# Kernel tuning notes

Measured on AMD Instinct MI355X. Metric: run time of the kernel, lower is better.

The kernel has to match this reference:

```python
import jax, jax.numpy as jnp
import numpy as np

B, N, K = 256, 1024, 64          # batch, atoms per structure, abc combinations
E = 2 * K                        # embedding_dim = 128
NSG = 230                        # number of space groups
LN_EPS = 1e-5


def setup_inputs() -> dict:
    key = jax.random.key(0)
    ks = jax.random.split(key, 12)
    xav = float(np.sqrt(6.0 / (K + K)))  # xavier_uniform bound for [K,K] slices
    return {
        "atom_positions": jax.random.uniform(ks[0], (B, N, 3), dtype=jnp.float32),
        "reciprocal_matrices": jax.random.normal(ks[1], (B, 3, 3), dtype=jnp.float32),
        "space_group": jax.random.randint(ks[2], (B, 1), 1, NSG + 1, dtype=jnp.int32),
        "abc_combinations": jax.random.normal(ks[3], (K, 3), dtype=jnp.float32),
        "graphs_array": jax.random.uniform(ks[4], (NSG, K, K), dtype=jnp.float32),
        "w_real": jax.random.uniform(ks[5], (NSG, K, K), jnp.float32, -xav, xav),
        "w_imag": jax.random.uniform(ks[6], (NSG, K, K), jnp.float32, -xav, xav),
        "b_real": jnp.zeros((NSG, K), jnp.float32),
        "b_imag": jnp.zeros((NSG, K), jnp.float32),
        "W2": jax.random.normal(ks[7], (E, E), dtype=jnp.float32) * 0.05,
        "b2": jnp.zeros((E,), jnp.float32),
        "gamma": jnp.ones((E,), jnp.float32),
        "beta": jnp.zeros((E,), jnp.float32),
    }


def reference(atom_positions, reciprocal_matrices, space_group, abc_combinations,
              graphs_array, w_real, w_imag, b_real, b_imag, W2, b2, gamma, beta):
    sg = space_group[:, 0] - 1                                  # [B] in [0,229]
    # transformed_abc = abc @ recip^T : [B,K,3]
    t_abc = jnp.einsum('kc,bdc->bkd', abc_combinations, reciprocal_matrices)
    # encodings = exp(i*2pi * pos @ t_abc^T) : [B,N,K] complex
    phase = (2.0 * jnp.pi) * jnp.einsum('bnc,bkc->bnk', atom_positions, t_abc)
    enc = jax.lax.complex(jnp.cos(phase), jnp.sin(phase))
    # per-sample adjacency gather + complex batched matmul
    adj = graphs_array[sg]                                      # [B,K,K]
    weighted = jnp.einsum('bnk,bkm->bnm', enc, adj.astype(enc.dtype))
    weighted = weighted[:, :, :K]                               # slice to embedding_dim//2
    # SpaceGroupDenseLayer: per-sample complex expert weights
    Wc = jax.lax.complex(w_real, w_imag)[sg]                    # [B,K,K]
    bc = jax.lax.complex(b_real, b_imag)[sg][:, None, :]        # [B,1,K]
    out_c = jnp.einsum('bni,bif->bnf', weighted, Wc) + bc       # [B,N,K] complex
    x = jnp.concatenate([out_c.real, out_c.imag], axis=-1)      # [B,N,2K]
    x = jax.nn.silu(x)
    x = x @ W2.T + b2                                           # Linear(E,E)
    mu = jnp.mean(x, axis=-1, keepdims=True)
    var = jnp.mean(jnp.square(x - mu), axis=-1, keepdims=True)
    return (x - mu) * jax.lax.rsqrt(var + LN_EPS) * gamma + beta
```

## Files before the change

### kernel.cpp

```cpp
#include <hip/hip_runtime.h>
#include <math.h>

#define BB 256
#define NN 1024
#define KK 64
#define EE 128
#define TM 128

typedef _Float16 half8 __attribute__((ext_vector_type(8)));
typedef float f32x4 __attribute__((ext_vector_type(4)));

__device__ __forceinline__ int swz(int row, int halfcol) {
    return (row * EE + halfcol) ^ ((row & 7) << 3);
}
__device__ __forceinline__ int swzX(int row, int halfcol) {
    return (row * EE + halfcol) ^ (((row >> 2) & 3) << 4);
}

__device__ __forceinline__ void gload_lds16(const void* g, void* l) {
    __builtin_amdgcn_global_load_lds(
        (const __attribute__((address_space(1))) unsigned int*)g,
        (__attribute__((address_space(3))) unsigned int*)l, 16, 0, 0);
}

__global__ __launch_bounds__(256) void prep_kernel(
    const float* __restrict__ recip,
    const int* __restrict__ space_group,
    const float* __restrict__ abc,
    const float* __restrict__ graphs,
    const float* __restrict__ w_real,
    const float* __restrict__ w_imag,
    const float* __restrict__ b_real,
    const float* __restrict__ b_imag,
    const float* __restrict__ W2,
    _Float16* __restrict__ Mt,
    float* __restrict__ bbout,
    float* __restrict__ tabcP,
    _Float16* __restrict__ W2h)
{
    const int b = blockIdx.x;
    const int t = threadIdx.x;
    const int sg = space_group[b] - 1;

    if (b < EE * EE / 256) {
        const int idx = b * 256 + t;
        W2h[idx] = (_Float16)W2[idx];
    }

    __shared__ float adjL[KK * KK];
    __shared__ float wrL[KK * KK];
    __shared__ float wiL[KK * KK];

    const float* adjG = graphs + (size_t)sg * KK * KK;
    const float* wrG  = w_real + (size_t)sg * KK * KK;
    const float* wiG  = w_imag + (size_t)sg * KK * KK;
    for (int idx = t; idx < KK * KK; idx += 256) {
        adjL[idx] = adjG[idx];
        wrL[idx]  = wrG[idx];
        wiL[idx]  = wiG[idx];
    }
    __syncthreads();

    const int i  = t >> 2;
    const int f0 = (t & 3) * 16;
    float cr[16], ci[16];
#pragma unroll
    for (int c = 0; c < 16; ++c) { cr[c] = 0.f; ci[c] = 0.f; }
    for (int k = 0; k < KK; ++k) {
        const float a = adjL[i * KK + k];
#pragma unroll
        for (int c = 0; c < 16; ++c) {
            cr[c] += a * wrL[k * KK + f0 + c];
            ci[c] += a * wiL[k * KK + f0 + c];
        }
    }
    _Float16* Mb = Mt + (size_t)b * EE * EE;
#pragma unroll
    for (int c = 0; c < 16; ++c) {
        const int f = f0 + c;
        Mb[f * EE + i]             = (_Float16)cr[c];
        Mb[f * EE + KK + i]        = (_Float16)(-ci[c]);
        Mb[(KK + f) * EE + i]      = (_Float16)ci[c];
        Mb[(KK + f) * EE + KK + i] = (_Float16)cr[c];
    }
    if (t < EE) {
        bbout[b * EE + t] = (t < KK) ? b_real[sg * KK + t] : b_imag[sg * KK + (t - KK)];
    }
    if (t < KK) {
        const float a0 = abc[t * 3 + 0], a1 = abc[t * 3 + 1], a2 = abc[t * 3 + 2];
        const float* R = recip + b * 9;
        float4 v;
        v.x = a0 * R[0] + a1 * R[1] + a2 * R[2];
        v.y = a0 * R[3] + a1 * R[4] + a2 * R[5];
        v.z = a0 * R[6] + a1 * R[7] + a2 * R[8];
        v.w = 0.f;
        *(float4*)&tabcP[((size_t)b * KK + t) * 4] = v;
    }
}

__global__ __launch_bounds__(512, 4) void main_kernel(
    const float* __restrict__ pos,
    const _Float16* __restrict__ Mt,
    const float* __restrict__ bball,
    const float* __restrict__ tabcP,
    const _Float16* __restrict__ W2h,
    const float* __restrict__ b2,
    const float* __restrict__ gamma,
    const float* __restrict__ beta,
    float* __restrict__ out)
{
    const int d = blockIdx.x;
    const int j   = d >> 3;
    const int b   = (d & 7) * 32 + (j >> 3);
    const int seg = j & 7;
    const int n0  = seg * TM;
    const int t  = threadIdx.x;
    const int w    = t >> 6;
    const int lane = t & 63;
    const int ln15 = lane & 15;
    const int kg   = lane >> 4;

    __shared__ __align__(16) _Float16 arena[2 * EE * EE];
    _Float16* Bt = arena;
    _Float16* X  = arena + EE * EE;

    {
        const char* srcM = (const char*)(Mt + (size_t)b * EE * EE);
#pragma unroll
        for (int i = 0; i < 4; ++i) {
            const int c16 = t + i * 512;
            const int row = c16 >> 4;
            const int sl  = c16 & 15;
            const int g   = row * 16 + (sl ^ (row & 7));
            gload_lds16(srcM + g * 16, (char*)Bt + c16 * 16);
        }
    }

    const int grow = n0 + w * 16 + ln15;
    const float* pr = pos + ((size_t)b * NN + grow) * 3;
    const float px = pr[0], py = pr[1], pz = pr[2];
    const float* tp = tabcP + (size_t)b * KK * 4;

    half8 afrag[4];
#pragma unroll
    for (int mq = 0; mq < 2; ++mq) {
        _Float16 cb[8], sb[8];
#pragma unroll
        for (int jj = 0; jj < 8; ++jj) {
            const int k = mq * 32 + kg * 8 + jj;
            const float4 tv = *(const float4*)&tp[k * 4];
            const float rev = px * tv.x + py * tv.y + pz * tv.z;
            const float fr  = __builtin_amdgcn_fractf(rev);
            sb[jj] = (_Float16)__builtin_amdgcn_sinf(fr);
            cb[jj] = (_Float16)__builtin_amdgcn_cosf(fr);
        }
        afrag[mq]     = *(half8*)cb;
        afrag[mq + 2] = *(half8*)sb;
    }
    __syncthreads();

    f32x4 acc[8];
#pragma unroll
    for (int nt = 0; nt < 8; ++nt) {
        const int n = nt * 16 + ln15;
        f32x4 a = {0.f, 0.f, 0.f, 0.f};
#pragma unroll
        for (int kc = 0; kc < 4; ++kc) {
            const half8 bf = *(const half8*)&Bt[swz(n, kc * 32 + kg * 8)];
            a = __builtin_amdgcn_mfma_f32_16x16x32_f16(afrag[kc], bf, a, 0, 0, 0);
        }
        acc[nt] = a;
    }
    __syncthreads();

    {
        const char* srcW = (const char*)W2h;
#pragma unroll
        for (int i = 0; i < 4; ++i) {
            const int c16 = t + i * 512;
            const int row = c16 >> 4;
            const int sl  = c16 & 15;
            const int g   = row * 16 + (sl ^ (row & 7));
            gload_lds16(srcW + g * 16, (char*)Bt + c16 * 16);
        }
    }

#pragma unroll
    for (int nt = 0; nt < 8; ++nt) {
        const int col = nt * 16 + ln15;
        const float bbv = bball[b * EE + col];
#pragma unroll
        for (int r2 = 0; r2 < 4; ++r2) {
            const float v = acc[nt][r2] + bbv;
            const int rr = w * 16 + kg * 4 + r2;
            X[swzX(rr, col)] = (_Float16)(v / (1.f + __expf(-v)));
        }
    }

    const int arow = w * 16 + ln15;
    half8 a2[4];
#pragma unroll
    for (int kc = 0; kc < 4; ++kc)
        a2[kc] = *(const half8*)&X[swzX(arow, kc * 32 + kg * 8)];
    __syncthreads();

    f32x4 acc2[8];
#pragma unroll
    for (int nt = 0; nt < 8; ++nt) {
        const int n = nt * 16 + ln15;
        f32x4 a = {0.f, 0.f, 0.f, 0.f};
#pragma unroll
        for (int kc = 0; kc < 4; ++kc) {
            const half8 bf = *(const half8*)&Bt[swz(n, kc * 32 + kg * 8)];
            a = __builtin_amdgcn_mfma_f32_16x16x32_f16(a2[kc], bf, a, 0, 0, 0);
        }
        acc2[nt] = a;
    }

    float s[4] = {0.f, 0.f, 0.f, 0.f}, q[4] = {0.f, 0.f, 0.f, 0.f};
#pragma unroll
    for (int nt = 0; nt < 8; ++nt) {
        const int col = nt * 16 + ln15;
        const float b2v = b2[col];
#pragma unroll
        for (int r2 = 0; r2 < 4; ++r2) {
            const float v = acc2[nt][r2] + b2v;
            acc2[nt][r2] = v;
            s[r2] += v;
            q[r2] += v * v;
        }
    }
#pragma unroll
    for (int m = 1; m < 16; m <<= 1) {
#pragma unroll
        for (int r2 = 0; r2 < 4; ++r2) {
            s[r2] += __shfl_xor(s[r2], m);
            q[r2] += __shfl_xor(q[r2], m);
        }
    }
    const float inv = 1.f / EE;
    float mu[4], rs[4];
#pragma unroll
    for (int r2 = 0; r2 < 4; ++r2) {
        mu[r2] = s[r2] * inv;
        rs[r2] = rsqrtf(fmaxf(q[r2] * inv - mu[r2] * mu[r2], 0.f) + 1e-5f);
    }
#pragma unroll
    for (int nt = 0; nt < 8; ++nt) {
        const int col = nt * 16 + ln15;
        const float g  = gamma[col];
        const float be = beta[col];
#pragma unroll
        for (int r2 = 0; r2 < 4; ++r2) {
            const int rr = w * 16 + kg * 4 + r2;
            __builtin_nontemporal_store(
                (acc2[nt][r2] - mu[r2]) * rs[r2] * g + be,
                &out[((size_t)b * NN + n0 + rr) * EE + col]);
        }
    }
}

extern "C" void kernel_launch(void* const* d_in, const int* in_sizes, int n_in,
                              void* d_out, int out_size, void* d_ws, size_t ws_size,
                              hipStream_t stream) {
    const float* pos    = (const float*)d_in[0];
    const float* recip  = (const float*)d_in[1];
    const int*   sgp    = (const int*)d_in[2];
    const float* abc    = (const float*)d_in[3];
    const float* graphs = (const float*)d_in[4];
    const float* wr     = (const float*)d_in[5];
    const float* wi     = (const float*)d_in[6];
    const float* br     = (const float*)d_in[7];
    const float* bi     = (const float*)d_in[8];
    const float* W2     = (const float*)d_in[9];
    const float* b2     = (const float*)d_in[10];
    const float* gm     = (const float*)d_in[11];
    const float* bt     = (const float*)d_in[12];
    float* out = (float*)d_out;

    char* ws = (char*)d_ws;
    _Float16* Mt    = (_Float16*)ws;
    char* p = ws + (size_t)BB * EE * EE * 2;
    _Float16* W2h   = (_Float16*)p;            p += EE * EE * 2;
    float*    bball = (float*)p;               p += (size_t)BB * EE * 4;
    float*    tabcP = (float*)p;

    hipLaunchKernelGGL(prep_kernel, dim3(BB), dim3(256), 0, stream,
                       recip, sgp, abc, graphs, wr, wi, br, bi, W2, Mt, bball, tabcP, W2h);
    hipLaunchKernelGGL(main_kernel, dim3(BB * NN / TM), dim3(512), 0, stream,
                       pos, Mt, bball, tabcP, W2h, b2, gm, bt, out);
}
```

Baseline: 76.43 us.

## Split fused kernel into two matmul kernels with global fp16 intermediate

Splits the fused encoding+matmul+SiLU+matmul+LayerNorm kernel into two kernels that exchange the SiLU output through a 64 MB fp16 workspace buffer. The old fused kernel is kept as a fallback when the workspace is too small. This reduces per-kernel LDS and register pressure and removes the mid-kernel barrier with its W2 reload. The cost is a full extra global write and read of the intermediate, plus one more launch. It also changes the X swizzle and replaces the nontemporal output stores with plain stores.

```diff
diff --git a/kernel.cpp b/kernel.cpp
--- a/kernel.cpp
+++ b/kernel.cpp
@@ -12,9 +12,6 @@
 
 __device__ __forceinline__ int swz(int row, int halfcol) {
     return (row * EE + halfcol) ^ ((row & 7) << 3);
-}
-__device__ __forceinline__ int swzX(int row, int halfcol) {
-    return (row * EE + halfcol) ^ (((row >> 2) & 3) << 4);
 }
 
 __device__ __forceinline__ void gload_lds16(const void* g, void* l) {
@@ -98,7 +95,188 @@
     }
 }
 
-__global__ __launch_bounds__(512, 4) void main_kernel(
+__device__ __forceinline__ void block_map(int d, int& b, int& n0) {
+    const int j = d >> 3;
+    b  = (d & 7) * 32 + (j >> 3);
+    n0 = (j & 7) * TM;
+}
+
+__device__ __forceinline__ void make_afrag(const float* tp, float px, float py, float pz,
+                                           int kg, half8 afrag[4]) {
+#pragma unroll
+    for (int mq = 0; mq < 2; ++mq) {
+        _Float16 cb[8], sb[8];
+#pragma unroll
+        for (int jj = 0; jj < 8; ++jj) {
+            const int k = mq * 32 + kg * 8 + jj;
+            const float4 tv = *(const float4*)&tp[k * 4];
+            const float rev = px * tv.x + py * tv.y + pz * tv.z;
+            const float fr  = __builtin_amdgcn_fractf(rev);
+            sb[jj] = (_Float16)__builtin_amdgcn_sinf(fr);
+            cb[jj] = (_Float16)__builtin_amdgcn_cosf(fr);
+        }
+        afrag[mq]     = *(half8*)cb;
+        afrag[mq + 2] = *(half8*)sb;
+    }
+}
+
+__global__ __launch_bounds__(512) void mm1_kernel(
+    const float* __restrict__ pos,
+    const _Float16* __restrict__ Mt,
+    const float* __restrict__ bball,
+    const float* __restrict__ tabcP,
+    _Float16* __restrict__ Xg)
+{
+    int b, n0;
+    block_map(blockIdx.x, b, n0);
+    const int t  = threadIdx.x;
+    const int w    = t >> 6;
+    const int lane = t & 63;
+    const int ln15 = lane & 15;
+    const int kg   = lane >> 4;
+
+    __shared__ __align__(16) _Float16 Bt[EE * EE];
+
+    {
+        const char* srcM = (const char*)(Mt + (size_t)b * EE * EE);
+#pragma unroll
+        for (int i = 0; i < 4; ++i) {
+            const int c16 = t + i * 512;
+            const int row = c16 >> 4;
+            const int sl  = c16 & 15;
+            const int g   = row * 16 + (sl ^ (row & 7));
+            gload_lds16(srcM + g * 16, (char*)Bt + c16 * 16);
+        }
+    }
+
+    const int grow = n0 + w * 16 + ln15;
+    const float* pr = pos + ((size_t)b * NN + grow) * 3;
+    const float px = pr[0], py = pr[1], pz = pr[2];
+    half8 afrag[4];
+    make_afrag(tabcP + (size_t)b * KK * 4, px, py, pz, kg, afrag);
+    __syncthreads();
+
+    f32x4 acc[8];
+#pragma unroll
+    for (int nt = 0; nt < 8; ++nt) {
+        const int n = nt * 16 + ln15;
+        f32x4 a = {0.f, 0.f, 0.f, 0.f};
+#pragma unroll
+        for (int kc = 0; kc < 4; ++kc) {
+            const half8 bf = *(const half8*)&Bt[swz(n, kc * 32 + kg * 8)];
+            a = __builtin_amdgcn_mfma_f32_16x16x32_f16(afrag[kc], bf, a, 0, 0, 0);
+        }
+        acc[nt] = a;
+    }
+
+#pragma unroll
+    for (int nt = 0; nt < 8; ++nt) {
+        const int col = nt * 16 + ln15;
+        const float bbv = bball[b * EE + col];
+#pragma unroll
+        for (int r2 = 0; r2 < 4; ++r2) {
+            const float v = acc[nt][r2] + bbv;
+            const int rr = w * 16 + kg * 4 + r2;
+            Xg[((size_t)b * NN + n0 + rr) * EE + col] =
+                (_Float16)(v / (1.f + __expf(-v)));
+        }
+    }
+}
+
+__global__ __launch_bounds__(512) void mm2_kernel(
+    const _Float16* __restrict__ Xg,
+    const _Float16* __restrict__ W2h,
+    const float* __restrict__ b2,
+    const float* __restrict__ gamma,
+    const float* __restrict__ beta,
+    float* __restrict__ out)
+{
+    int b, n0;
+    block_map(blockIdx.x, b, n0);
+    const int t  = threadIdx.x;
+    const int w    = t >> 6;
+    const int lane = t & 63;
+    const int ln15 = lane & 15;
+    const int kg   = lane >> 4;
+
+    __shared__ __align__(16) _Float16 Bt[EE * EE];
+
+    const int grow = n0 + w * 16 + ln15;
+    const _Float16* xrow = Xg + ((size_t)b * NN + grow) * EE;
+    half8 a2[4];
+#pragma unroll
+    for (int kc = 0; kc < 4; ++kc)
+        a2[kc] = *(const half8*)&xrow[kc * 32 + kg * 8];
+
+    {
+        const char* srcW = (const char*)W2h;
+#pragma unroll
+        for (int i = 0; i < 4; ++i) {
+            const int c16 = t + i * 512;
+            const int row = c16 >> 4;
+            const int sl  = c16 & 15;
+            const int g   = row * 16 + (sl ^ (row & 7));
+            gload_lds16(srcW + g * 16, (char*)Bt + c16 * 16);
+        }
+    }
+    __syncthreads();
+
+    f32x4 acc2[8];
+#pragma unroll
+    for (int nt = 0; nt < 8; ++nt) {
+        const int n = nt * 16 + ln15;
+        f32x4 a = {0.f, 0.f, 0.f, 0.f};
+#pragma unroll
+        for (int kc = 0; kc < 4; ++kc) {
+            const half8 bf = *(const half8*)&Bt[swz(n, kc * 32 + kg * 8)];
+            a = __builtin_amdgcn_mfma_f32_16x16x32_f16(a2[kc], bf, a, 0, 0, 0);
+        }
+        acc2[nt] = a;
+    }
+
+    float s[4] = {0.f, 0.f, 0.f, 0.f}, q[4] = {0.f, 0.f, 0.f, 0.f};
+#pragma unroll
+    for (int nt = 0; nt < 8; ++nt) {
+        const int col = nt * 16 + ln15;
+        const float b2v = b2[col];
+#pragma unroll
+        for (int r2 = 0; r2 < 4; ++r2) {
+            const float v = acc2[nt][r2] + b2v;
+            acc2[nt][r2] = v;
+            s[r2] += v;
+            q[r2] += v * v;
+        }
+    }
+#pragma unroll
+    for (int m = 1; m < 16; m <<= 1) {
+#pragma unroll
+        for (int r2 = 0; r2 < 4; ++r2) {
+            s[r2] += __shfl_xor(s[r2], m);
+            q[r2] += __shfl_xor(q[r2], m);
+        }
+    }
+    const float inv = 1.f / EE;
+    float mu[4], rs[4];
+#pragma unroll
+    for (int r2 = 0; r2 < 4; ++r2) {
+        mu[r2] = s[r2] * inv;
+        rs[r2] = rsqrtf(fmaxf(q[r2] * inv - mu[r2] * mu[r2], 0.f) + 1e-5f);
+    }
+#pragma unroll
+    for (int nt = 0; nt < 8; ++nt) {
+        const int col = nt * 16 + ln15;
+        const float g  = gamma[col];
+        const float be = beta[col];
+#pragma unroll
+        for (int r2 = 0; r2 < 4; ++r2) {
+            const int rr = w * 16 + kg * 4 + r2;
+            out[((size_t)b * NN + n0 + rr) * EE + col] =
+                (acc2[nt][r2] - mu[r2]) * rs[r2] * g + be;
+        }
+    }
+}
+
+__global__ __launch_bounds__(512, 4) void fused_kernel(
     const float* __restrict__ pos,
     const _Float16* __restrict__ Mt,
     const float* __restrict__ bball,
@@ -109,11 +287,8 @@
     const float* __restrict__ beta,
     float* __restrict__ out)
 {
-    const int d = blockIdx.x;
-    const int j   = d >> 3;
-    const int b   = (d & 7) * 32 + (j >> 3);
-    const int seg = j & 7;
-    const int n0  = seg * TM;
+    int b, n0;
+    block_map(blockIdx.x, b, n0);
     const int t  = threadIdx.x;
     const int w    = t >> 6;
     const int lane = t & 63;
@@ -135,28 +310,11 @@
             gload_lds16(srcM + g * 16, (char*)Bt + c16 * 16);
         }
     }
-
     const int grow = n0 + w * 16 + ln15;
     const float* pr = pos + ((size_t)b * NN + grow) * 3;
     const float px = pr[0], py = pr[1], pz = pr[2];
-    const float* tp = tabcP + (size_t)b * KK * 4;
-
     half8 afrag[4];
-#pragma unroll
-    for (int mq = 0; mq < 2; ++mq) {
-        _Float16 cb[8], sb[8];
-#pragma unroll
-        for (int jj = 0; jj < 8; ++jj) {
-            const int k = mq * 32 + kg * 8 + jj;
-            const float4 tv = *(const float4*)&tp[k * 4];
-            const float rev = px * tv.x + py * tv.y + pz * tv.z;
-            const float fr  = __builtin_amdgcn_fractf(rev);
-            sb[jj] = (_Float16)__builtin_amdgcn_sinf(fr);
-            cb[jj] = (_Float16)__builtin_amdgcn_cosf(fr);
-        }
-        afrag[mq]     = *(half8*)cb;
-        afrag[mq + 2] = *(half8*)sb;
-    }
+    make_afrag(tabcP + (size_t)b * KK * 4, px, py, pz, kg, afrag);
     __syncthreads();
 
     f32x4 acc[8];
@@ -184,7 +342,6 @@
             gload_lds16(srcW + g * 16, (char*)Bt + c16 * 16);
         }
     }
-
 #pragma unroll
     for (int nt = 0; nt < 8; ++nt) {
         const int col = nt * 16 + ln15;
@@ -193,15 +350,14 @@
         for (int r2 = 0; r2 < 4; ++r2) {
             const float v = acc[nt][r2] + bbv;
             const int rr = w * 16 + kg * 4 + r2;
-            X[swzX(rr, col)] = (_Float16)(v / (1.f + __expf(-v)));
-        }
-    }
-
+            X[swz(rr, col)] = (_Float16)(v / (1.f + __expf(-v)));
+        }
+    }
     const int arow = w * 16 + ln15;
     half8 a2[4];
 #pragma unroll
     for (int kc = 0; kc < 4; ++kc)
-        a2[kc] = *(const half8*)&X[swzX(arow, kc * 32 + kg * 8)];
+        a2[kc] = *(const half8*)&X[swz(arow, kc * 32 + kg * 8)];
     __syncthreads();
 
     f32x4 acc2[8];
@@ -253,9 +409,8 @@
 #pragma unroll
         for (int r2 = 0; r2 < 4; ++r2) {
             const int rr = w * 16 + kg * 4 + r2;
-            __builtin_nontemporal_store(
-                (acc2[nt][r2] - mu[r2]) * rs[r2] * g + be,
-                &out[((size_t)b * NN + n0 + rr) * EE + col]);
+            out[((size_t)b * NN + n0 + rr) * EE + col] =
+                (acc2[nt][r2] - mu[r2]) * rs[r2] * g + be;
         }
     }
 }
@@ -283,10 +438,19 @@
     char* p = ws + (size_t)BB * EE * EE * 2;
     _Float16* W2h   = (_Float16*)p;            p += EE * EE * 2;
     float*    bball = (float*)p;               p += (size_t)BB * EE * 4;
-    float*    tabcP = (float*)p;
+    float*    tabcP = (float*)p;               p += (size_t)BB * KK * 16;
+    _Float16* Xg    = (_Float16*)p;
+    const size_t need = (size_t)(p - ws) + (size_t)BB * NN * EE * 2;
 
     hipLaunchKernelGGL(prep_kernel, dim3(BB), dim3(256), 0, stream,
                        recip, sgp, abc, graphs, wr, wi, br, bi, W2, Mt, bball, tabcP, W2h);
-    hipLaunchKernelGGL(main_kernel, dim3(BB * NN / TM), dim3(512), 0, stream,
-                       pos, Mt, bball, tabcP, W2h, b2, gm, bt, out);
-}
+    if (ws_size >= need) {
+        hipLaunchKernelGGL(mm1_kernel, dim3(BB * NN / TM), dim3(512), 0, stream,
+                           pos, Mt, bball, tabcP, Xg);
+        hipLaunchKernelGGL(mm2_kernel, dim3(BB * NN / TM), dim3(512), 0, stream,
+                           Xg, W2h, b2, gm, bt, out);
+    } else {
+        hipLaunchKernelGGL(fused_kernel, dim3(BB * NN / TM), dim3(512), 0, stream,
+                           pos, Mt, bball, tabcP, W2h, b2, gm, bt, out);
+    }
+}
```

Measured after the change: 87.52 us. 1.15x slower.
